# Optimization experiments

Measured on AMD Instinct MI355X. Metric: run time of the kernel, lower is better.

## Reference

```python
import jax, jax.numpy as jnp
import numpy as np

N_GOOD = 16
NUM_TEST = 16
NUM_UNITS = 32
EPS = 1e-5


def _mlp(x, w1, b1, w2, b2):
    # Linear -> ReLU -> Linear -> ReLU
    h = jax.nn.relu(x @ w1 + b1)
    return jax.nn.relu(h @ w2 + b2)


def _ln_relu(x, g, b):
    mu = jnp.mean(x, axis=-1, keepdims=True)
    var = jnp.mean(jnp.square(x - mu), axis=-1, keepdims=True)
    return jax.nn.relu((x - mu) / jnp.sqrt(var + EPS) * g + b)


def _attend(self_out, enc):
    # self_out: [B, D], enc: [B, N, D]
    scores = jnp.einsum('bd,bnd->bn', self_out, enc) / np.float32(np.sqrt(NUM_TEST))
    attn = jax.nn.softmax(scores, axis=-1)
    return jnp.einsum('bn,bnd->bd', attn, enc)


def setup_inputs() -> dict:
    key = jax.random.key(0)
    ks = jax.random.split(key, 24)
    B = 262144
    obs_dim = 4 + (N_GOOD - 1) * 5 + N_GOOD * 3  # 127

    def lin(k, fan_in, fan_out):
        bound = 1.0 / np.sqrt(fan_in)
        kw, kb = jax.random.split(k)
        w = jax.random.uniform(kw, (fan_in, fan_out), jnp.float32, -bound, bound)
        b = jax.random.uniform(kb, (fan_out,), jnp.float32, -bound, bound)
        return w, b

    en_w1, en_b1 = lin(ks[0], 4, NUM_UNITS)
    en_w2, en_b2 = lin(ks[1], NUM_UNITS, NUM_TEST)
    oa_w1, oa_b1 = lin(ks[2], 5, NUM_UNITS)
    oa_w2, oa_b2 = lin(ks[3], NUM_UNITS, NUM_TEST)
    g_w1, g_b1 = lin(ks[4], 3, NUM_UNITS)
    g_w2, g_b2 = lin(ks[5], NUM_UNITS, NUM_TEST)
    m_w1, m_b1 = lin(ks[6], NUM_TEST * 3, NUM_UNITS)
    m_w2, m_b2 = lin(ks[7], NUM_UNITS, NUM_UNITS)
    m_w3, m_b3 = lin(ks[8], NUM_UNITS, 2)

    return {
        's_input': jax.random.normal(ks[9], (B, obs_dim), jnp.float32),
        'en_w1': en_w1, 'en_b1': en_b1, 'en_w2': en_w2, 'en_b2': en_b2,
        'oa_w1': oa_w1, 'oa_b1': oa_b1, 'oa_w2': oa_w2, 'oa_b2': oa_b2,
        'oa_g': jnp.ones((NUM_TEST,), jnp.float32), 'oa_bln': jnp.zeros((NUM_TEST,), jnp.float32),
        'g_w1': g_w1, 'g_b1': g_b1, 'g_w2': g_w2, 'g_b2': g_b2,
        'g_g': jnp.ones((NUM_TEST,), jnp.float32), 'g_bln': jnp.zeros((NUM_TEST,), jnp.float32),
        'm_w1': m_w1, 'm_b1': m_b1, 'm_w2': m_w2, 'm_b2': m_b2, 'm_w3': m_w3, 'm_b3': m_b3,
    }


def reference(s_input, en_w1, en_b1, en_w2, en_b2,
              oa_w1, oa_b1, oa_w2, oa_b2, oa_g, oa_bln,
              g_w1, g_b1, g_w2, g_b2, g_g, g_bln,
              m_w1, m_b1, m_w2, m_b2, m_w3, m_b3):
    n = N_GOOD
    B = s_input.shape[0]

    # self encoding: [B, 16]
    self_out = _mlp(s_input[:, :4], en_w1, en_b1, en_w2, en_b2)

    # other agents: width (n-1)*5 = [pos pairs | vel pairs | scalar per agent]
    og = s_input[:, 4:4 + (n - 1) * 5]
    pos = og[:, :(n - 1) * 2].reshape(B, n - 1, 2)
    vel = og[:, (n - 1) * 2:(n - 1) * 4].reshape(B, n - 1, 2)
    scal = og[:, (n - 1) * 4:(n - 1) * 5].reshape(B, n - 1, 1)
    other_in = jnp.concatenate([pos, vel, scal], axis=-1)  # [B, n-1, 5]
    other_enc = _mlp(other_in, oa_w1, oa_b1, oa_w2, oa_b2)  # [B, n-1, 16]
    other_out = _ln_relu(_attend(self_out, other_enc), oa_g, oa_bln)

    # food/goals: last n*3 cols, chunks of 3
    food_in = s_input[:, -n * 3:].reshape(B, n, 3)
    food_enc = _mlp(food_in, g_w1, g_b1, g_w2, g_b2)  # [B, n, 16]
    food_out = _ln_relu(_attend(self_out, food_enc), g_g, g_bln)

    merged = jnp.concatenate([self_out, food_out, other_out], axis=1)  # [B, 48]
    h = jax.nn.leaky_relu(merged @ m_w1 + m_b1, 0.01)
    h = jax.nn.leaky_relu(h @ m_w2 + m_b2, 0.01)
    return jnp.tanh(h @ m_w3 + m_b3)  # [B, 2]
```

## Files before the change

kernel.cpp:

```cpp
#include <hip/hip_runtime.h>
#include <math.h>


#define OBS 127
#define XSS 132

typedef _Float16 v4h  __attribute__((ext_vector_type(4)));
typedef _Float16 v8h  __attribute__((ext_vector_type(8)));
typedef __fp16   p2h  __attribute__((ext_vector_type(2)));
typedef float    v16f __attribute__((ext_vector_type(16)));
typedef float    f4u  __attribute__((ext_vector_type(4), aligned(4)));

#define MFMA16(a, b, c) __builtin_amdgcn_mfma_f32_32x32x16_f16((a), (b), (c), 0, 0, 0)

union PK8 { p2h p[4]; v8h h; };
union HU8 { unsigned u[4]; v8h h; _Float16 e[8]; };

__device__ __forceinline__ v8h zero8h() {
    v8h z;
    #pragma unroll
    for (int j = 0; j < 8; ++j) z[j] = (_Float16)0.f;
    return z;
}
__device__ __forceinline__ v8h pk8(const v16f& d, int b) {
    PK8 q;
    q.p[0] = __builtin_amdgcn_cvt_pkrtz(d[b],     d[b + 1]);
    q.p[1] = __builtin_amdgcn_cvt_pkrtz(d[b + 2], d[b + 3]);
    q.p[2] = __builtin_amdgcn_cvt_pkrtz(d[b + 4], d[b + 5]);
    q.p[3] = __builtin_amdgcn_cvt_pkrtz(d[b + 6], d[b + 7]);
    return q.h;
}
__device__ __forceinline__ v8h pkr8(const v16f& d, int b) {
    return __builtin_elementwise_max(pk8(d, b), zero8h());
}
__device__ __forceinline__ v8h pk8f(const float (&v)[8]) {
    PK8 q;
    q.p[0] = __builtin_amdgcn_cvt_pkrtz(v[0], v[1]);
    q.p[1] = __builtin_amdgcn_cvt_pkrtz(v[2], v[3]);
    q.p[2] = __builtin_amdgcn_cvt_pkrtz(v[4], v[5]);
    q.p[3] = __builtin_amdgcn_cvt_pkrtz(v[6], v[7]);
    return q.h;
}
__device__ __forceinline__ v8h lrelu8(v8h t) {
    const v8h s = t * (_Float16)0.01f;
    return __builtin_elementwise_max(t, s);
}
__device__ __forceinline__ v8h a1fragK16(const float* __restrict__ W,
                                         const float* __restrict__ b,
                                         int kin, int m, int h) {
    const int Lm = (m & ~12) | ((m & 4) << 1) | ((m & 8) >> 1);
    v8h r;
    #pragma unroll
    for (int j = 0; j < 8; ++j) {
        const int k = 8 * h + j;
        const float v = (k < kin) ? W[k * 32 + Lm] : (k == kin ? b[Lm] : 0.f);
        r[j] = (_Float16)v;
    }
    return r;
}
__device__ __forceinline__ v8h a2fragK16(const float* __restrict__ W2,
                                         int s, int m, int h) {
    v8h r;
    #pragma unroll
    for (int j = 0; j < 8; ++j)
        r[j] = (_Float16)((m < 16) ? W2[(16 * s + 8 * h + j) * 16 + m] : 0.f);
    return r;
}
__device__ __forceinline__ v8h mfragK16(const float* __restrict__ W, int ncols,
                                        int base, int m, int h, int colmax) {
    v8h r;
    #pragma unroll
    for (int j = 0; j < 8; ++j) {
        const int ch = base + (j & 3) + 8 * (j >> 2) + 4 * h;
        r[j] = (_Float16)((m < colmax) ? W[ch * ncols + m] : 0.f);
    }
    return r;
}
__device__ __forceinline__ float fast_tanh(float x) {
    x = fminf(fmaxf(x, -15.f), 15.f);
    const float ex = __expf(2.f * x);
    return (ex - 1.f) / (ex + 1.f);
}

template <int BR>
__device__ __forceinline__ void entity_step(const _Float16* __restrict__ xr,
                                            int e, int h,
                                            v8h A1, v8h A2a, v8h A2b,
                                            const float (&b2v)[8],
                                            const float (&stl)[8],
                                            float& l, float (&o)[8],
                                            v16f z16) {
    v8h bf = zero8h();
    if (h == 0) {
        HU8 u;
        #pragma unroll
        for (int j = 0; j < 4; ++j) u.u[j] = 0;
        if (BR == 1) {
            u.e[0] = xr[79 + 3 * e];
            u.e[1] = xr[80 + 3 * e];
            u.e[2] = xr[81 + 3 * e];
            u.e[3] = (_Float16)1.f;
        } else {
            u.u[0] = *(const unsigned*)(xr + 4 + 2 * e);
            u.u[1] = *(const unsigned*)(xr + 34 + 2 * e);
            u.e[4] = xr[64 + e];
            u.e[5] = (_Float16)1.f;
        }
        bf = u.h;
    }
    const v16f dH = MFMA16(A1, bf, z16);
    const v8h p0 = pkr8(dH, 0);
    const v8h p1 = pkr8(dH, 8);
    v16f c = MFMA16(A2a, p0, z16);
    c = MFMA16(A2b, p1, c);
    float e2[8], part = 0.f;
    #pragma unroll
    for (int r = 0; r < 8; ++r) {
        e2[r] = fmaxf(c[r] + b2v[r], 0.f);
        part += stl[r] * e2[r];
    }
    part += __shfl_xor(part, 32);
    const float p = __builtin_amdgcn_exp2f(part);
    l += p;
    #pragma unroll
    for (int r = 0; r < 8; ++r) o[r] += p * e2[r];
}

__device__ __forceinline__ v8h ln_fin(float l, const float (&o)[8],
                                      const float (&gv)[8], const float (&blv)[8]) {
    const float rl = 1.f / l;
    float a[8], sum = 0.f;
    #pragma unroll
    for (int r = 0; r < 8; ++r) { a[r] = o[r] * rl; sum += a[r]; }
    sum += __shfl_xor(sum, 32);
    const float mu = sum * 0.0625f;
    float var = 0.f;
    #pragma unroll
    for (int r = 0; r < 8; ++r) { a[r] -= mu; var += a[r] * a[r]; }
    var += __shfl_xor(var, 32);
    const float inv = rsqrtf(var * 0.0625f + 1e-5f);
    float v[8];
    #pragma unroll
    for (int r = 0; r < 8; ++r) v[r] = fmaxf(a[r] * inv * gv[r] + blv[r], 0.f);
    return pk8f(v);
}

__global__ __launch_bounds__(256)
void actor_mfma(const float* __restrict__ x,
                const float* __restrict__ en_w1, const float* __restrict__ en_b1,
                const float* __restrict__ en_w2, const float* __restrict__ en_b2,
                const float* __restrict__ oa_w1, const float* __restrict__ oa_b1,
                const float* __restrict__ oa_w2, const float* __restrict__ oa_b2,
                const float* __restrict__ oa_g,  const float* __restrict__ oa_bln,
                const float* __restrict__ g_w1,  const float* __restrict__ g_b1,
                const float* __restrict__ g_w2,  const float* __restrict__ g_b2,
                const float* __restrict__ g_g,   const float* __restrict__ g_bln,
                const float* __restrict__ m_w1,  const float* __restrict__ m_b1,
                const float* __restrict__ m_w2,  const float* __restrict__ m_b2,
                const float* __restrict__ m_w3,  const float* __restrict__ m_b3,
                float* __restrict__ out, int B)
{
    const int lane = threadIdx.x & 63, wid = threadIdx.x >> 6;
    const int n = lane & 31, h = lane >> 5;

    __shared__ __align__(16) _Float16 xs_all[4][32 * XSS];
    _Float16* xs = xs_all[wid];

    const int r0 = blockIdx.x * 128 + wid * 32;
    const bool wvalid = (r0 < B);

    if (wvalid) {
        const float* __restrict__ xp = x + (size_t)r0 * OBS;
        if (r0 + 32 <= B) {
            #pragma unroll
            for (int i = 0; i < 16; ++i) {
                const int gI = i * 64 + lane;
                if (gI < 992) {
                    const int row = gI / 31;
                    const int c4 = gI - row * 31;
                    const f4u v = *(const f4u*)(xp + row * 127 + c4 * 4);
                    PK8 q;
                    q.p[0] = __builtin_amdgcn_cvt_pkrtz(v[0], v[1]);
                    q.p[1] = __builtin_amdgcn_cvt_pkrtz(v[2], v[3]);
                    *(uint2*)(xs + row * XSS + c4 * 4) = *(const uint2*)&q;
                }
            }
            #pragma unroll
            for (int t = 0; t < 2; ++t) {
                const int idx = t * 64 + lane;
                if (idx < 96) {
                    const int row = idx / 3;
                    const int c = 124 + idx - row * 3;
                    xs[row * XSS + c] = (_Float16)xp[row * 127 + c];
                }
            }
        } else {
            const int lim = (B - r0) * OBS;
            for (int i = 0; i < 64; ++i) {
                const int f = i * 64 + lane;
                if (f < lim) {
                    const int r = f / 127;
                    xs[f + 5 * r] = (_Float16)xp[f];
                }
            }
        }
    }
    __syncthreads();

    v16f z16;
    #pragma unroll
    for (int r = 0; r < 16; ++r) z16[r] = 0.f;

    float sb2v[8], fb2v[8], ob2v[8];
    #pragma unroll
    for (int r = 0; r < 8; ++r) {
        const int m = (r & 3) + 8 * (r >> 2) + 4 * h;
        sb2v[r] = en_b2[m];
        fb2v[r] = g_b2[m];
        ob2v[r] = oa_b2[m];
    }

    const _Float16* xr = xs + n * XSS;
    float st[8], stl[8];
    v8h Bs;
    {
        const v8h sA1 = a1fragK16(en_w1, en_b1, 4, n, h);
        const v8h sA2a = a2fragK16(en_w2, 0, n, h);
        const v8h sA2b = a2fragK16(en_w2, 1, n, h);
        v8h bs = zero8h();
        if (h == 0) {
            HU8 u;
            #pragma unroll
            for (int j = 0; j < 4; ++j) u.u[j] = 0;
            *(uint2*)&u.u[0] = *(const uint2*)xr;
            u.e[4] = (_Float16)1.f;
            bs = u.h;
        }
        const v16f dS = MFMA16(sA1, bs, z16);
        v16f cS = MFMA16(sA2a, pkr8(dS, 0), z16);
        cS = MFMA16(sA2b, pkr8(dS, 8), cS);
        const float SK = 0.25f * 1.44269504088896f;
        float sv[8];
        #pragma unroll
        for (int r = 0; r < 8; ++r) {
            sv[r] = fmaxf(cS[r] + sb2v[r], 0.f);
            st[r] = sv[r];
            stl[r] = sv[r] * SK;
        }
        Bs = pk8f(sv);
    }

    const v8h fA1 = a1fragK16(g_w1, g_b1, 3, n, h);
    const v8h fA2a = a2fragK16(g_w2, 0, n, h);
    const v8h fA2b = a2fragK16(g_w2, 1, n, h);
    const v8h oA1 = a1fragK16(oa_w1, oa_b1, 5, n, h);
    const v8h oA2a = a2fragK16(oa_w2, 0, n, h);
    const v8h oA2b = a2fragK16(oa_w2, 1, n, h);

    float lf = 0.f, lo = 0.f, of[8], oo[8];
    #pragma unroll
    for (int r = 0; r < 8; ++r) { of[r] = 0.f; oo[r] = 0.f; }
    #pragma unroll 2
    for (int e = 0; e < 16; ++e) {
        entity_step<1>(xr, e, h, fA1, fA2a, fA2b, fb2v, stl, lf, of, z16);
        if (e < 15)
            entity_step<0>(xr, e, h, oA1, oA2a, oA2b, ob2v, stl, lo, oo, z16);
    }

    float fgv[8], fblv[8], ogv[8], oblv[8];
    #pragma unroll
    for (int r = 0; r < 8; ++r) {
        const int m = (r & 3) + 8 * (r >> 2) + 4 * h;
        fgv[r] = g_g[m];  fblv[r] = g_bln[m];
        ogv[r] = oa_g[m]; oblv[r] = oa_bln[m];
    }
    const v8h Bf = ln_fin(lf, of, fgv, fblv);
    const v8h Bo = ln_fin(lo, oo, ogv, oblv);

    v16f m1C, m2C;
    #pragma unroll
    for (int r = 0; r < 16; ++r) {
        const int m = (r & 3) + 8 * (r >> 2) + 4 * h;
        m1C[r] = m_b1[m];
        m2C[r] = m_b2[m];
    }
    v16f m1 = MFMA16(mfragK16(m_w1, 32, 0, n, h, 32), Bs, m1C);
    m1 = MFMA16(mfragK16(m_w1, 32, 16, n, h, 32), Bf, m1);
    m1 = MFMA16(mfragK16(m_w1, 32, 32, n, h, 32), Bo, m1);
    const v8h q0 = lrelu8(pk8(m1, 0));
    const v8h q1 = lrelu8(pk8(m1, 8));
    v16f m2 = MFMA16(mfragK16(m_w2, 32, 0, n, h, 32), q0, m2C);
    m2 = MFMA16(mfragK16(m_w2, 32, 16, n, h, 32), q1, m2);
    const v8h z0 = lrelu8(pk8(m2, 0));
    const v8h z1 = lrelu8(pk8(m2, 8));
    v16f m3 = MFMA16(mfragK16(m_w3, 2, 0, n, h, 2), z0, z16);
    m3 = MFMA16(mfragK16(m_w3, 2, 16, n, h, 2), z1, m3);

    if (h == 0 && wvalid && r0 + n < B) {
        float2 res;
        res.x = fast_tanh(m3[0] + m_b3[0]);
        res.y = fast_tanh(m3[1] + m_b3[1]);
        *(float2*)(out + (size_t)(r0 + n) * 2) = res;
    }
}

extern "C" void kernel_launch(void* const* d_in, const int* in_sizes, int n_in,
                              void* d_out, int out_size, void* d_ws, size_t ws_size,
                              hipStream_t stream) {
    const int B = in_sizes[0] / OBS;
    const float* xin = (const float*)d_in[0];
    const float* en_w1 = (const float*)d_in[1];
    const float* en_b1 = (const float*)d_in[2];
    const float* en_w2 = (const float*)d_in[3];
    const float* en_b2 = (const float*)d_in[4];
    const float* oa_w1 = (const float*)d_in[5];
    const float* oa_b1 = (const float*)d_in[6];
    const float* oa_w2 = (const float*)d_in[7];
    const float* oa_b2 = (const float*)d_in[8];
    const float* oa_g  = (const float*)d_in[9];
    const float* oa_bl = (const float*)d_in[10];
    const float* g_w1  = (const float*)d_in[11];
    const float* g_b1  = (const float*)d_in[12];
    const float* g_w2  = (const float*)d_in[13];
    const float* g_b2  = (const float*)d_in[14];
    const float* g_g   = (const float*)d_in[15];
    const float* g_bl  = (const float*)d_in[16];
    const float* m_w1  = (const float*)d_in[17];
    const float* m_b1  = (const float*)d_in[18];
    const float* m_w2  = (const float*)d_in[19];
    const float* m_b2  = (const float*)d_in[20];
    const float* m_w3  = (const float*)d_in[21];
    const float* m_b3  = (const float*)d_in[22];

    const int rows_per_block = 128;
    const int grid = (B + rows_per_block - 1) / rows_per_block;
    actor_mfma<<<grid, 256, 0, stream>>>(
        xin, en_w1, en_b1, en_w2, en_b2,
        oa_w1, oa_b1, oa_w2, oa_b2, oa_g, oa_bl,
        g_w1, g_b1, g_w2, g_b2, g_g, g_bl,
        m_w1, m_b1, m_w2, m_b2, m_w3, m_b3,
        (float*)d_out, B);
}
```

Baseline: 298.0 us.

## Split food and other-agent attention branches across two waves per 32-row tile

Each 32-row tile is now handled by a 128-thread block of two waves instead of one wave doing both branches. Both waves load the shared input tile and redundantly compute the self encoding. Wave 0 runs the 16-entity food branch and wave 1 runs the 15-entity other-agent branch, each with two independent accumulator chains to expose more instruction-level parallelism. Wave 1 passes its layer-norm output through shared memory after a block barrier so wave 0 can run the merge MLP. This shortens each wave's serial chain but duplicates the self-encoding work, adds a barrier, and leaves wave 1 idle during the tail.

Result: slower. 324.1 us (+8.7%).

```diff
diff --git a/kernel.cpp b/kernel.cpp
--- a/kernel.cpp
+++ b/kernel.cpp
@@ -15,6 +15,7 @@
 
 union PK8 { p2h p[4]; v8h h; };
 union HU8 { unsigned u[4]; v8h h; _Float16 e[8]; };
+union BO  { v8h h; uint4 u; };
 
 __device__ __forceinline__ v8h zero8h() {
     v8h z;
@@ -145,7 +146,7 @@
     return pk8f(v);
 }
 
-__global__ __launch_bounds__(256)
+__global__ __launch_bounds__(128)
 void actor_mfma(const float* __restrict__ x,
                 const float* __restrict__ en_w1, const float* __restrict__ en_b1,
                 const float* __restrict__ en_w2, const float* __restrict__ en_b2,
@@ -163,44 +164,41 @@
     const int lane = threadIdx.x & 63, wid = threadIdx.x >> 6;
     const int n = lane & 31, h = lane >> 5;
 
-    __shared__ __align__(16) _Float16 xs_all[4][32 * XSS];
-    _Float16* xs = xs_all[wid];
-
-    const int r0 = blockIdx.x * 128 + wid * 32;
-    const bool wvalid = (r0 < B);
-
-    if (wvalid) {
-        const float* __restrict__ xp = x + (size_t)r0 * OBS;
-        if (r0 + 32 <= B) {
+    __shared__ __align__(16) _Float16 xs[32 * XSS];
+    __shared__ __align__(16) uint4 bobuf[64];
+
+    const int r0 = blockIdx.x * 32;
+
+    {
+        const int rs = r0 + 16 * wid;
+        const float* __restrict__ xp = x + (size_t)rs * OBS;
+        _Float16* xw = xs + 16 * wid * XSS;
+        if (rs + 16 <= B) {
             #pragma unroll
-            for (int i = 0; i < 16; ++i) {
+            for (int i = 0; i < 8; ++i) {
                 const int gI = i * 64 + lane;
-                if (gI < 992) {
+                if (gI < 496) {
                     const int row = gI / 31;
                     const int c4 = gI - row * 31;
                     const f4u v = *(const f4u*)(xp + row * 127 + c4 * 4);
                     PK8 q;
                     q.p[0] = __builtin_amdgcn_cvt_pkrtz(v[0], v[1]);
                     q.p[1] = __builtin_amdgcn_cvt_pkrtz(v[2], v[3]);
-                    *(uint2*)(xs + row * XSS + c4 * 4) = *(const uint2*)&q;
+                    *(uint2*)(xw + row * XSS + c4 * 4) = *(const uint2*)&q;
                 }
             }
-            #pragma unroll
-            for (int t = 0; t < 2; ++t) {
-                const int idx = t * 64 + lane;
-                if (idx < 96) {
-                    const int row = idx / 3;
-                    const int c = 124 + idx - row * 3;
-                    xs[row * XSS + c] = (_Float16)xp[row * 127 + c];
-                }
+            if (lane < 48) {
+                const int row = lane / 3;
+                const int c = 124 + lane - row * 3;
+                xw[row * XSS + c] = (_Float16)xp[row * 127 + c];
             }
-        } else {
-            const int lim = (B - r0) * OBS;
-            for (int i = 0; i < 64; ++i) {
+        } else if (rs < B) {
+            const int lim = (B - rs) * OBS;
+            for (int i = 0; i < 32; ++i) {
                 const int f = i * 64 + lane;
                 if (f < lim) {
                     const int r = f / 127;
-                    xs[f + 5 * r] = (_Float16)xp[f];
+                    xw[f + 5 * r] = (_Float16)xp[f];
                 }
             }
         }
@@ -211,13 +209,11 @@
     #pragma unroll
     for (int r = 0; r < 16; ++r) z16[r] = 0.f;
 
-    float sb2v[8], fb2v[8], ob2v[8];
+    float sb2v[8];
     #pragma unroll
     for (int r = 0; r < 8; ++r) {
         const int m = (r & 3) + 8 * (r >> 2) + 4 * h;
         sb2v[r] = en_b2[m];
-        fb2v[r] = g_b2[m];
-        ob2v[r] = oa_b2[m];
     }
 
     const _Float16* xr = xs + n * XSS;
@@ -250,57 +246,88 @@
         Bs = pk8f(sv);
     }
 
-    const v8h fA1 = a1fragK16(g_w1, g_b1, 3, n, h);
-    const v8h fA2a = a2fragK16(g_w2, 0, n, h);
-    const v8h fA2b = a2fragK16(g_w2, 1, n, h);
-    const v8h oA1 = a1fragK16(oa_w1, oa_b1, 5, n, h);
-    const v8h oA2a = a2fragK16(oa_w2, 0, n, h);
-    const v8h oA2b = a2fragK16(oa_w2, 1, n, h);
-
-    float lf = 0.f, lo = 0.f, of[8], oo[8];
-    #pragma unroll
-    for (int r = 0; r < 8; ++r) { of[r] = 0.f; oo[r] = 0.f; }
-    #pragma unroll 2
-    for (int e = 0; e < 16; ++e) {
-        entity_step<1>(xr, e, h, fA1, fA2a, fA2b, fb2v, stl, lf, of, z16);
-        if (e < 15)
-            entity_step<0>(xr, e, h, oA1, oA2a, oA2b, ob2v, stl, lo, oo, z16);
-    }
-
-    float fgv[8], fblv[8], ogv[8], oblv[8];
-    #pragma unroll
-    for (int r = 0; r < 8; ++r) {
-        const int m = (r & 3) + 8 * (r >> 2) + 4 * h;
-        fgv[r] = g_g[m];  fblv[r] = g_bln[m];
-        ogv[r] = oa_g[m]; oblv[r] = oa_bln[m];
-    }
-    const v8h Bf = ln_fin(lf, of, fgv, fblv);
-    const v8h Bo = ln_fin(lo, oo, ogv, oblv);
-
-    v16f m1C, m2C;
-    #pragma unroll
-    for (int r = 0; r < 16; ++r) {
-        const int m = (r & 3) + 8 * (r >> 2) + 4 * h;
-        m1C[r] = m_b1[m];
-        m2C[r] = m_b2[m];
-    }
-    v16f m1 = MFMA16(mfragK16(m_w1, 32, 0, n, h, 32), Bs, m1C);
-    m1 = MFMA16(mfragK16(m_w1, 32, 16, n, h, 32), Bf, m1);
-    m1 = MFMA16(mfragK16(m_w1, 32, 32, n, h, 32), Bo, m1);
-    const v8h q0 = lrelu8(pk8(m1, 0));
-    const v8h q1 = lrelu8(pk8(m1, 8));
-    v16f m2 = MFMA16(mfragK16(m_w2, 32, 0, n, h, 32), q0, m2C);
-    m2 = MFMA16(mfragK16(m_w2, 32, 16, n, h, 32), q1, m2);
-    const v8h z0 = lrelu8(pk8(m2, 0));
-    const v8h z1 = lrelu8(pk8(m2, 8));
-    v16f m3 = MFMA16(mfragK16(m_w3, 2, 0, n, h, 2), z0, z16);
-    m3 = MFMA16(mfragK16(m_w3, 2, 16, n, h, 2), z1, m3);
-
-    if (h == 0 && wvalid && r0 + n < B) {
-        float2 res;
-        res.x = fast_tanh(m3[0] + m_b3[0]);
-        res.y = fast_tanh(m3[1] + m_b3[1]);
-        *(float2*)(out + (size_t)(r0 + n) * 2) = res;
+    v8h Bf = zero8h();
+    if (wid == 1) {
+        const v8h oA1 = a1fragK16(oa_w1, oa_b1, 5, n, h);
+        const v8h oA2a = a2fragK16(oa_w2, 0, n, h);
+        const v8h oA2b = a2fragK16(oa_w2, 1, n, h);
+        float ob2v[8], ogv[8], oblv[8];
+        #pragma unroll
+        for (int r = 0; r < 8; ++r) {
+            const int m = (r & 3) + 8 * (r >> 2) + 4 * h;
+            ob2v[r] = oa_b2[m];
+            ogv[r] = oa_g[m]; oblv[r] = oa_bln[m];
+        }
+        float l0 = 0.f, l1 = 0.f, o0[8], o1[8];
+        #pragma unroll
+        for (int r = 0; r < 8; ++r) { o0[r] = 0.f; o1[r] = 0.f; }
+        #pragma unroll 2
+        for (int i = 0; i < 7; ++i) {
+            entity_step<0>(xr, 2 * i,     h, oA1, oA2a, oA2b, ob2v, stl, l0, o0, z16);
+            entity_step<0>(xr, 2 * i + 1, h, oA1, oA2a, oA2b, ob2v, stl, l1, o1, z16);
+        }
+        entity_step<0>(xr, 14, h, oA1, oA2a, oA2b, ob2v, stl, l0, o0, z16);
+        l0 += l1;
+        #pragma unroll
+        for (int r = 0; r < 8; ++r) o0[r] += o1[r];
+        BO bo;
+        bo.h = ln_fin(l0, o0, ogv, oblv);
+        bobuf[lane] = bo.u;
+    } else {
+        const v8h fA1 = a1fragK16(g_w1, g_b1, 3, n, h);
+        const v8h fA2a = a2fragK16(g_w2, 0, n, h);
+        const v8h fA2b = a2fragK16(g_w2, 1, n, h);
+        float fb2v[8], fgv[8], fblv[8];
+        #pragma unroll
+        for (int r = 0; r < 8; ++r) {
+            const int m = (r & 3) + 8 * (r >> 2) + 4 * h;
+            fb2v[r] = g_b2[m];
+            fgv[r] = g_g[m]; fblv[r] = g_bln[m];
+        }
+        float l0 = 0.f, l1 = 0.f, o0[8], o1[8];
+        #pragma unroll
+        for (int r = 0; r < 8; ++r) { o0[r] = 0.f; o1[r] = 0.f; }
+        #pragma unroll 2
+        for (int i = 0; i < 8; ++i) {
+            entity_step<1>(xr, 2 * i,     h, fA1, fA2a, fA2b, fb2v, stl, l0, o0, z16);
+            entity_step<1>(xr, 2 * i + 1, h, fA1, fA2a, fA2b, fb2v, stl, l1, o1, z16);
+        }
+        l0 += l1;
+        #pragma unroll
+        for (int r = 0; r < 8; ++r) o0[r] += o1[r];
+        Bf = ln_fin(l0, o0, fgv, fblv);
+    }
+    __syncthreads();
+
+    if (wid == 0) {
+        BO bo;
+        bo.u = bobuf[lane];
+        const v8h Bo = bo.h;
+        v16f m1C, m2C;
+        #pragma unroll
+        for (int r = 0; r < 16; ++r) {
+            const int m = (r & 3) + 8 * (r >> 2) + 4 * h;
+            m1C[r] = m_b1[m];
+            m2C[r] = m_b2[m];
+        }
+        v16f m1 = MFMA16(mfragK16(m_w1, 32, 0, n, h, 32), Bs, m1C);
+        m1 = MFMA16(mfragK16(m_w1, 32, 16, n, h, 32), Bf, m1);
+        m1 = MFMA16(mfragK16(m_w1, 32, 32, n, h, 32), Bo, m1);
+        const v8h q0 = lrelu8(pk8(m1, 0));
+        const v8h q1 = lrelu8(pk8(m1, 8));
+        v16f m2 = MFMA16(mfragK16(m_w2, 32, 0, n, h, 32), q0, m2C);
+        m2 = MFMA16(mfragK16(m_w2, 32, 16, n, h, 32), q1, m2);
+        const v8h z0 = lrelu8(pk8(m2, 0));
+        const v8h z1 = lrelu8(pk8(m2, 8));
+        v16f m3 = MFMA16(mfragK16(m_w3, 2, 0, n, h, 2), z0, z16);
+        m3 = MFMA16(mfragK16(m_w3, 2, 16, n, h, 2), z1, m3);
+
+        if (h == 0 && r0 + n < B) {
+            float2 res;
+            res.x = fast_tanh(m3[0] + m_b3[0]);
+            res.y = fast_tanh(m3[1] + m_b3[1]);
+            *(float2*)(out + (size_t)(r0 + n) * 2) = res;
+        }
     }
 }
 
@@ -332,9 +359,8 @@
     const float* m_w3  = (const float*)d_in[21];
     const float* m_b3  = (const float*)d_in[22];
 
-    const int rows_per_block = 128;
-    const int grid = (B + rows_per_block - 1) / rows_per_block;
-    actor_mfma<<<grid, 256, 0, stream>>>(
+    const int grid = (B + 31) / 32;
+    actor_mfma<<<grid, 128, 0, stream>>>(
         xin, en_w1, en_b1, en_w2, en_b2,
         oa_w1, oa_b1, oa_w2, oa_b2, oa_g, oa_bl,
         g_w1, g_b1, g_w2, g_b2, g_g, g_bl,
```

## Shrink LDS staging, load self features directly, fold bias into MFMA accumulators

Applied to the files above, without the earlier changes.

The shared-memory row stride drops from 132 to 124 halves because the first four self-input columns are no longer staged. Each lane instead reads its row's self features straight from global memory into registers. The second-layer biases are now fed as the MFMA accumulator init rather than added afterwards, removing per-element adds. Launch bounds now request 5 blocks per SM, which raises occupancy but may cause register spills.

Result: slower. 519.1 us (+74.2%).

```diff
diff --git a/kernel.cpp b/kernel.cpp
--- a/kernel.cpp
+++ b/kernel.cpp
@@ -3,7 +3,7 @@
 
 
 #define OBS 127
-#define XSS 132
+#define XSS 124
 
 typedef _Float16 v4h  __attribute__((ext_vector_type(4)));
 typedef _Float16 v8h  __attribute__((ext_vector_type(8)));
@@ -76,6 +76,20 @@
     }
     return r;
 }
+__device__ __forceinline__ v16f biasC8(const float* __restrict__ b, int h) {
+    v16f c;
+    #pragma unroll
+    for (int r = 0; r < 8; ++r) c[r] = b[(r & 3) + 8 * (r >> 2) + 4 * h];
+    #pragma unroll
+    for (int r = 8; r < 16; ++r) c[r] = 0.f;
+    return c;
+}
+__device__ __forceinline__ v16f biasC16(const float* __restrict__ b, int h) {
+    v16f c;
+    #pragma unroll
+    for (int r = 0; r < 16; ++r) c[r] = b[(r & 3) + 8 * (r >> 2) + 4 * h];
+    return c;
+}
 __device__ __forceinline__ float fast_tanh(float x) {
     x = fminf(fmaxf(x, -15.f), 15.f);
     const float ex = __expf(2.f * x);
@@ -86,7 +100,7 @@
 __device__ __forceinline__ void entity_step(const _Float16* __restrict__ xr,
                                             int e, int h,
                                             v8h A1, v8h A2a, v8h A2b,
-                                            const float (&b2v)[8],
+                                            const v16f& b2C,
                                             const float (&stl)[8],
                                             float& l, float (&o)[8],
                                             v16f z16) {
@@ -96,14 +110,14 @@
         #pragma unroll
         for (int j = 0; j < 4; ++j) u.u[j] = 0;
         if (BR == 1) {
-            u.e[0] = xr[79 + 3 * e];
-            u.e[1] = xr[80 + 3 * e];
-            u.e[2] = xr[81 + 3 * e];
+            u.e[0] = xr[75 + 3 * e];
+            u.e[1] = xr[76 + 3 * e];
+            u.e[2] = xr[77 + 3 * e];
             u.e[3] = (_Float16)1.f;
         } else {
-            u.u[0] = *(const unsigned*)(xr + 4 + 2 * e);
-            u.u[1] = *(const unsigned*)(xr + 34 + 2 * e);
-            u.e[4] = xr[64 + e];
+            u.u[0] = *(const unsigned*)(xr + 2 * e);
+            u.u[1] = *(const unsigned*)(xr + 30 + 2 * e);
+            u.e[4] = xr[60 + e];
             u.e[5] = (_Float16)1.f;
         }
         bf = u.h;
@@ -111,12 +125,12 @@
     const v16f dH = MFMA16(A1, bf, z16);
     const v8h p0 = pkr8(dH, 0);
     const v8h p1 = pkr8(dH, 8);
-    v16f c = MFMA16(A2a, p0, z16);
+    v16f c = MFMA16(A2a, p0, b2C);
     c = MFMA16(A2b, p1, c);
     float e2[8], part = 0.f;
     #pragma unroll
     for (int r = 0; r < 8; ++r) {
-        e2[r] = fmaxf(c[r] + b2v[r], 0.f);
+        e2[r] = fmaxf(c[r], 0.f);
         part += stl[r] * e2[r];
     }
     part += __shfl_xor(part, 32);
@@ -145,7 +159,7 @@
     return pk8f(v);
 }
 
-__global__ __launch_bounds__(256)
+__global__ __launch_bounds__(256, 5)
 void actor_mfma(const float* __restrict__ x,
                 const float* __restrict__ en_w1, const float* __restrict__ en_b1,
                 const float* __restrict__ en_w2, const float* __restrict__ en_b2,
@@ -169,20 +183,26 @@
     const int r0 = blockIdx.x * 128 + wid * 32;
     const bool wvalid = (r0 < B);
 
+    f4u selfv;
+    #pragma unroll
+    for (int j = 0; j < 4; ++j) selfv[j] = 0.f;
+    if (wvalid && r0 + n < B)
+        selfv = *(const f4u*)(x + (size_t)(r0 + n) * OBS);
+
     if (wvalid) {
         const float* __restrict__ xp = x + (size_t)r0 * OBS;
         if (r0 + 32 <= B) {
             #pragma unroll
-            for (int i = 0; i < 16; ++i) {
+            for (int i = 0; i < 15; ++i) {
                 const int gI = i * 64 + lane;
-                if (gI < 992) {
-                    const int row = gI / 31;
-                    const int c4 = gI - row * 31;
-                    const f4u v = *(const f4u*)(xp + row * 127 + c4 * 4);
+                {
+                    const int row = gI / 30;
+                    const int c4 = gI - row * 30;
+                    const f4u v = *(const f4u*)(xp + row * 127 + 4 + 4 * c4);
                     PK8 q;
                     q.p[0] = __builtin_amdgcn_cvt_pkrtz(v[0], v[1]);
                     q.p[1] = __builtin_amdgcn_cvt_pkrtz(v[2], v[3]);
-                    *(uint2*)(xs + row * XSS + c4 * 4) = *(const uint2*)&q;
+                    *(uint2*)(xs + row * XSS + 4 * c4) = *(const uint2*)&q;
                 }
             }
             #pragma unroll
@@ -190,18 +210,18 @@
                 const int idx = t * 64 + lane;
                 if (idx < 96) {
                     const int row = idx / 3;
-                    const int c = 124 + idx - row * 3;
-                    xs[row * XSS + c] = (_Float16)xp[row * 127 + c];
+                    const int c = idx - row * 3;
+                    xs[row * XSS + 120 + c] = (_Float16)xp[row * 127 + 124 + c];
                 }
             }
         } else {
-            const int lim = (B - r0) * OBS;
+            const int nrow = B - r0;
             for (int i = 0; i < 64; ++i) {
                 const int f = i * 64 + lane;
-                if (f < lim) {
-                    const int r = f / 127;
-                    xs[f + 5 * r] = (_Float16)xp[f];
-                }
+                const int row = f / 123;
+                const int c = f - row * 123;
+                if (row < nrow)
+                    xs[row * XSS + c] = (_Float16)xp[row * 127 + 4 + c];
             }
         }
     }
@@ -210,15 +230,6 @@
     v16f z16;
     #pragma unroll
     for (int r = 0; r < 16; ++r) z16[r] = 0.f;
-
-    float sb2v[8], fb2v[8], ob2v[8];
-    #pragma unroll
-    for (int r = 0; r < 8; ++r) {
-        const int m = (r & 3) + 8 * (r >> 2) + 4 * h;
-        sb2v[r] = en_b2[m];
-        fb2v[r] = g_b2[m];
-        ob2v[r] = oa_b2[m];
-    }
 
     const _Float16* xr = xs + n * XSS;
     float st[8], stl[8];
@@ -227,23 +238,27 @@
         const v8h sA1 = a1fragK16(en_w1, en_b1, 4, n, h);
         const v8h sA2a = a2fragK16(en_w2, 0, n, h);
         const v8h sA2b = a2fragK16(en_w2, 1, n, h);
+        const v16f sb2C = biasC8(en_b2, h);
         v8h bs = zero8h();
         if (h == 0) {
             HU8 u;
             #pragma unroll
             for (int j = 0; j < 4; ++j) u.u[j] = 0;
-            *(uint2*)&u.u[0] = *(const uint2*)xr;
+            PK8 q;
+            q.p[0] = __builtin_amdgcn_cvt_pkrtz(selfv[0], selfv[1]);
+            q.p[1] = __builtin_amdgcn_cvt_pkrtz(selfv[2], selfv[3]);
+            *(uint2*)&u.u[0] = *(const uint2*)&q;
             u.e[4] = (_Float16)1.f;
             bs = u.h;
         }
         const v16f dS = MFMA16(sA1, bs, z16);
-        v16f cS = MFMA16(sA2a, pkr8(dS, 0), z16);
+        v16f cS = MFMA16(sA2a, pkr8(dS, 0), sb2C);
         cS = MFMA16(sA2b, pkr8(dS, 8), cS);
         const float SK = 0.25f * 1.44269504088896f;
         float sv[8];
         #pragma unroll
         for (int r = 0; r < 8; ++r) {
-            sv[r] = fmaxf(cS[r] + sb2v[r], 0.f);
+            sv[r] = fmaxf(cS[r], 0.f);
             st[r] = sv[r];
             stl[r] = sv[r] * SK;
         }
@@ -256,15 +271,17 @@
     const v8h oA1 = a1fragK16(oa_w1, oa_b1, 5, n, h);
     const v8h oA2a = a2fragK16(oa_w2, 0, n, h);
     const v8h oA2b = a2fragK16(oa_w2, 1, n, h);
+    const v16f fb2C = biasC8(g_b2, h);
+    const v16f ob2C = biasC8(oa_b2, h);
 
     float lf = 0.f, lo = 0.f, of[8], oo[8];
     #pragma unroll
     for (int r = 0; r < 8; ++r) { of[r] = 0.f; oo[r] = 0.f; }
     #pragma unroll 2
     for (int e = 0; e < 16; ++e) {
-        entity_step<1>(xr, e, h, fA1, fA2a, fA2b, fb2v, stl, lf, of, z16);
+        entity_step<1>(xr, e, h, fA1, fA2a, fA2b, fb2C, stl, lf, of, z16);
         if (e < 15)
-            entity_step<0>(xr, e, h, oA1, oA2a, oA2b, ob2v, stl, lo, oo, z16);
+            entity_step<0>(xr, e, h, oA1, oA2a, oA2b, ob2C, stl, lo, oo, z16);
     }
 
     float fgv[8], fblv[8], ogv[8], oblv[8];
@@ -277,13 +294,8 @@
     const v8h Bf = ln_fin(lf, of, fgv, fblv);
     const v8h Bo = ln_fin(lo, oo, ogv, oblv);
 
-    v16f m1C, m2C;
-    #pragma unroll
-    for (int r = 0; r < 16; ++r) {
-        const int m = (r & 3) + 8 * (r >> 2) + 4 * h;
-        m1C[r] = m_b1[m];
-        m2C[r] = m_b2[m];
-    }
+    const v16f m1C = biasC16(m_b1, h);
+    const v16f m2C = biasC16(m_b2, h);
     v16f m1 = MFMA16(mfragK16(m_w1, 32, 0, n, h, 32), Bs, m1C);
     m1 = MFMA16(mfragK16(m_w1, 32, 16, n, h, 32), Bf, m1);
     m1 = MFMA16(mfragK16(m_w1, 32, 32, n, h, 32), Bo, m1);
```
